# Optimization experiments

Hardware: AMD Instinct MI355X
Metric: run time of the kernel (lower is better)

The kernel has to match this reference:

```python
import jax, jax.numpy as jnp
import numpy as np

# Model dims (match init_kwargs)
N_P, NV, P, S = 60, 5, 20, 14   # particles, vertices, pf features, sv features
HID, DE, DO, NCLS, BATCH = 60, 20, 24, 2, 512

# Rr/Rs one-hot matrices encode edges (r, s) for r != s with r varying slowest.
# So gather-by-Rr == repeat each node N-1 times, gather-by-Rs == index by senders,
# and scatter-sum by Rr^T == reshape to [B, N, N-1, De] and sum axis 2.
_SENDERS = np.array([s for r in range(N_P) for s in range(N_P) if s != r])


def _lin_params(key, din, dout):
    kw, kb = jax.random.split(key)
    bound = 1.0 / np.sqrt(din)
    w = jax.random.uniform(kw, (din, dout), minval=-bound, maxval=bound, dtype=jnp.float32)
    b = jax.random.uniform(kb, (dout,), minval=-bound, maxval=bound, dtype=jnp.float32)
    return w, b


def setup_inputs() -> dict:
    key = jax.random.key(0)
    ks = jax.random.split(key, 12)
    inp = {
        'x': jax.random.normal(ks[0], (BATCH, P, N_P), dtype=jnp.float32),
        'y': jax.random.normal(ks[1], (BATCH, S, NV), dtype=jnp.float32),
    }
    specs = [('fr', [(2 * P, HID), (HID, HID), (HID, DE)]),
             ('pv', [(S + P, HID), (HID, HID), (HID, DE)]),
             ('fo', [(P + 2 * DE, HID), (HID, HID), (HID, DO)])]
    ki = 2
    for name, dims in specs:
        for j, (di, do) in enumerate(dims, 1):
            w, b = _lin_params(ks[ki], di, do)
            ki += 1
            inp[f'{name}_w{j}'] = w
            inp[f'{name}_b{j}'] = b
    w, b = _lin_params(ks[11], DO, NCLS)
    inp['fc_w'] = w
    inp['fc_b'] = b
    return inp


def _mlp3(h, w1, b1, w2, b2, w3, b3):
    h = jax.nn.relu(h @ w1 + b1)
    h = jax.nn.relu(h @ w2 + b2)
    return jax.nn.relu(h @ w3 + b3)


def reference(x, y, fr_w1, fr_b1, fr_w2, fr_b2, fr_w3, fr_b3,
              pv_w1, pv_b1, pv_w2, pv_b2, pv_w3, pv_b3,
              fo_w1, fo_b1, fo_w2, fo_b2, fo_w3, fo_b3, fc_w, fc_b):
    xt = jnp.swapaxes(x, -1, -2)  # [B, N, P]
    yt = jnp.swapaxes(y, -1, -2)  # [B, Nv, S]
    B = xt.shape[0]

    # particle-particle edge conv (gather via index, scatter-sum via reshape)
    Orr = jnp.repeat(xt, N_P - 1, axis=1)          # [B, Nr, P], receiver features
    Ors = xt[:, _SENDERS]                          # [B, Nr, P], sender features
    E = _mlp3(jnp.concatenate([Orr, Ors], axis=-1),
              fr_w1, fr_b1, fr_w2, fr_b2, fr_w3, fr_b3)  # [B, Nr, De]
    Ebar_pp = E.reshape(B, N_P, N_P - 1, DE).sum(axis=2)  # [B, N, De]

    # particle-vertex edge conv (Rk repeats particles, Rv tiles vertices)
    Ork = jnp.repeat(xt, NV, axis=1)               # [B, Nt, P]
    Orv = jnp.tile(yt, (1, N_P, 1))                # [B, Nt, S]
    E2 = _mlp3(jnp.concatenate([Ork, Orv], axis=-1),
               pv_w1, pv_b1, pv_w2, pv_b2, pv_w3, pv_b3)  # [B, Nt, De]
    Ebar_pv = E2.reshape(B, N_P, NV, DE).sum(axis=2)      # [B, N, De]

    C = jnp.concatenate([xt, Ebar_pp, Ebar_pv], axis=-1)  # [B, N, P + 2*De]
    O = _mlp3(C, fo_w1, fo_b1, fo_w2, fo_b2, fo_w3, fo_b3)  # [B, N, Do]
    return O.sum(axis=-2) @ fc_w + fc_b  # [B, num_classes]
```

## Files before the change

### kernel.cpp

```cpp
#include <hip/hip_runtime.h>

#define BATCH 512
#define NPART 60
#define PFEAT 20
#define SFEAT 14
#define NVTX  5
#define HID   60
#define DE    20
#define DO    24
#define NCLS  2
#define SR    68

typedef _Float16 half8  __attribute__((ext_vector_type(8)));
typedef _Float16 half4v __attribute__((ext_vector_type(4)));
typedef __fp16   fp16x2 __attribute__((ext_vector_type(2)));
typedef float    f32x4  __attribute__((ext_vector_type(4)));

__device__ __forceinline__ half4v pkcvt4(f32x4 a) {
    fp16x2 lo = __builtin_amdgcn_cvt_pkrtz(a[0], a[1]);
    fp16x2 hi = __builtin_amdgcn_cvt_pkrtz(a[2], a[3]);
    half4v r;
    r[0] = (_Float16)lo[0]; r[1] = (_Float16)lo[1];
    r[2] = (_Float16)hi[0]; r[3] = (_Float16)hi[1];
    return r;
}
__device__ __forceinline__ half4v relu4(half4v a) {
#pragma unroll
    for (int j = 0; j < 4; ++j)
        a[j] = (a[j] > (_Float16)0.f) ? a[j] : (_Float16)0.f;
    return a;
}

__global__ __launch_bounds__(256) void prep_kernel(
    const float* __restrict__ x,
    const float* __restrict__ fr_w1, const float* __restrict__ fr_b1,
    const float* __restrict__ pv_w1,
    const float* __restrict__ fr_w2, const float* __restrict__ fr_b2,
    const float* __restrict__ fr_w3, const float* __restrict__ fr_b3,
    const float* __restrict__ pv_w2, const float* __restrict__ pv_b2,
    const float* __restrict__ pv_w3, const float* __restrict__ pv_b3,
    const float* __restrict__ fo_w1, const float* __restrict__ fo_b1,
    const float* __restrict__ fo_w2, const float* __restrict__ fo_b2,
    const float* __restrict__ fo_w3, const float* __restrict__ fo_b3,
    _Float16* __restrict__ frW2p, _Float16* __restrict__ frW3p16,
    _Float16* __restrict__ pvW2p, _Float16* __restrict__ pvW3p16,
    _Float16* __restrict__ foW1p, _Float16* __restrict__ foW2p16,
    _Float16* __restrict__ foW3p16,
    _Float16* __restrict__ frW1Ap, _Float16* __restrict__ frW1Bp,
    _Float16* __restrict__ pvW1Ap, _Float16* __restrict__ xp)
{
    if (blockIdx.x < 16) {
        int idx = blockIdx.x*256 + threadIdx.x;
        {
            int j  = idx & 7;
            int L  = (idx >> 3) & 63;
            int kk = (idx >> 9) & 1;
            int u  = idx >> 10;
            int k  = kk*32 + (L >> 4)*8 + j;
            int n  = u*16 + (L & 15);
            float v2f = 0.f, v2p = 0.f, v1o = 0.f;
            if (k < HID && n < HID) {
                v2f = fr_w2[k*HID + n];
                v2p = pv_w2[k*HID + n];
                v1o = fo_w1[k*HID + n];
            } else if (k == HID) {
                if (n < HID)      { v2f = fr_b2[n]; v2p = pv_b2[n]; v1o = fo_b1[n]; }
                else if (n == HID){ v2f = 1.f;      v2p = 1.f;      v1o = 1.f; }
            }
            frW2p[idx] = (_Float16)v2f;
            pvW2p[idx] = (_Float16)v2p;
            foW1p[idx] = (_Float16)v1o;
        }
        {
            int j  = idx & 3;
            int L  = (idx >> 2) & 63;
            int kt = (idx >> 8) & 3;
            int u  = idx >> 10;
            int k  = kt*16 + (L >> 4)*4 + j;
            int n  = u*16 + (L & 15);
            float v = 0.f;
            if (k < HID && n < HID)        v = fo_w2[k*HID + n];
            else if (k == HID) {
                if (n < HID)       v = fo_b2[n];
                else if (n == HID) v = 1.f;
            }
            foW2p16[idx] = (_Float16)v;
        }
        if (idx < 2048) {
            {
                int j  = idx & 3;
                int L  = (idx >> 2) & 63;
                int kt = (idx >> 8) & 3;
                int u  = idx >> 10;
                int k  = kt*16 + (L >> 4)*4 + j;
                int n  = u*16 + (L & 15);
                float vf = 0.f, vp = 0.f, vo = 0.f;
                if (k < HID) {
                    if (n < DE) { vf = fr_w3[k*DE + n]; vp = pv_w3[k*DE + n]; }
                    if (n < DO)   vo = fo_w3[k*DO + n];
                } else if (k == HID) {
                    if (n < DE) { vf = fr_b3[n]; vp = pv_b3[n]; }
                    if (n < DO)   vo = fo_w3 ? fo_b3[n] : 0.f;
                }
                frW3p16[idx] = (_Float16)vf;
                pvW3p16[idx] = (_Float16)vp;
                foW3p16[idx] = (_Float16)vo;
            }
            {
                int j = idx & 7;
                int L = (idx >> 3) & 63;
                int u = idx >> 9;
                int k = (L >> 4)*8 + j;
                int n = u*16 + (L & 15);
                float va = 0.f, vb = 0.f, vpv = 0.f;
                if (k < PFEAT && n < HID) {
                    va  = fr_w1[k*HID + n];
                    vb  = fr_w1[(PFEAT + k)*HID + n];
                    vpv = pv_w1[k*HID + n];
                } else if (k == PFEAT) {
                    if (n < HID)       va = fr_b1[n];
                    else if (n == HID) va = 1.f;
                }
                frW1Ap[idx] = (_Float16)va;
                frW1Bp[idx] = (_Float16)vb;
                pvW1Ap[idx] = (_Float16)vpv;
            }
        }
    } else {
        int idx = (blockIdx.x - 16)*256 + threadIdx.x;
        if (idx < BATCH*NPART*4) {
            int p = idx % NPART;
            int t = idx / NPART;
            int q = t & 3;
            int b = t >> 2;
            half8 v;
#pragma unroll
            for (int j = 0; j < 8; ++j) {
                int k = q*8 + j;
                float f = 0.f;
                if (k < PFEAT)       f = x[((size_t)b*PFEAT + k)*NPART + p];
                else if (k == PFEAT) f = 1.f;
                v[j] = (_Float16)f;
            }
            *(half8*)(xp + (size_t)idx*8) = v;
        }
    }
}

__global__ __launch_bounds__(512) void fused_kernel(
    const float* __restrict__ y,
    const float* __restrict__ pv_w1, const float* __restrict__ pv_b1,
    const float* __restrict__ fcw, const float* __restrict__ fcb,
    const half8*  __restrict__ frw2p, const half4v* __restrict__ frw3p16,
    const half8*  __restrict__ pvw2p, const half4v* __restrict__ pvw3p16,
    const half8*  __restrict__ fow1p, const half4v* __restrict__ fow2p16,
    const half4v* __restrict__ fow3p16,
    const half8*  __restrict__ frw1ap, const half8* __restrict__ frw1bp,
    const half8*  __restrict__ pvw1ap, const _Float16* __restrict__ xp,
    float* __restrict__ out)
{
    __shared__ __align__(16) _Float16 sFrA[NPART*SR];
    __shared__ __align__(16) _Float16 sFrB[NPART*SR];
    __shared__ __align__(16) _Float16 sPvA[NPART*SR];
    __shared__ __align__(16) _Float16 sPvV[NVTX*64];
    __shared__ __align__(16) _Float16 sEpp[NPART*DE];
    __shared__ __align__(16) _Float16 sEpvP[NVTX*NPART*DE];
    __shared__ __align__(16) float    sDsum[4][DO];
    _Float16* sCin = sFrA;

    const f32x4 z4 = {0.f, 0.f, 0.f, 0.f};

    int bb   = blockIdx.x;
    int wv   = threadIdx.x >> 6;
    int lane = threadIdx.x & 63;
    int ml   = lane & 15;
    int q    = lane >> 4;

    {
        int tile = wv & 3;
        int row  = 16*tile + ml;
        int rr   = (row < NPART) ? row : 0;
        half8 bX = *(const half8*)(xp + (((size_t)bb*4 + q)*NPART + rr)*8);
#pragma unroll
        for (int task = 0; task < 2; ++task) {
            const half8* Wt; _Float16* Ot;
            if (wv < 4) {
                if (task == 0) { Wt = frw1ap; Ot = sFrA; }
                else           { Wt = pvw1ap; Ot = sPvA; }
            } else {
                if (task == 1) break;
                Wt = frw1bp; Ot = sFrB;
            }
#pragma unroll
            for (int u = 0; u < 4; ++u) {
                half8 w8 = Wt[u*64 + lane];
                f32x4 acc = z4;
                acc = __builtin_amdgcn_mfma_f32_16x16x32_f16(w8, bX, acc, 0, 0, 0);
                if (row < NPART)
                    *(half4v*)(Ot + row*SR + u*16 + 4*q) = pkcvt4(acc);
            }
        }
        for (int idx = threadIdx.x; idx < NVTX*64; idx += 512) {
            int v = idx >> 6;
            int h = idx & 63;
            float a;
            if (h < HID) {
                a = pv_b1[h];
#pragma unroll
                for (int f = 0; f < SFEAT; ++f)
                    a += y[((size_t)bb*SFEAT + f)*NVTX + v] * pv_w1[(PFEAT + f)*HID + h];
            } else {
                a = (h == HID) ? 1.f : 0.f;
            }
            sPvV[idx] = (_Float16)a;
        }
    }
    __syncthreads();

    {
        half8  w2r[8];
        half4v w3r[8];
#pragma unroll
        for (int t = 0; t < 8; ++t) w2r[t] = frw2p[t*64 + lane];
#pragma unroll
        for (int t = 0; t < 8; ++t) w3r[t] = frw3p16[t*64 + lane];
#pragma unroll
        for (int t = 0; t < 8; ++t) {
            asm volatile("" : "+v"(w2r[t]));
            asm volatile("" : "+v"(w3r[t]));
        }
        float ok3[4];
#pragma unroll
        for (int i = 0; i < 4; ++i) ok3[i] = (4*q + i < 11) ? 1.f : 0.f;

        for (int r = wv; r < NPART; r += 8) {
            half8 u8k0 = *(const half8*)(sFrA + r*SR + q*8);
            half8 u8k1 = *(const half8*)(sFrA + r*SR + 32 + q*8);
            float s0 = 0.f, s1 = 0.f;

#pragma unroll
            for (int c = 0; c < 4; ++c) {
                int edge = 16*c + ml;
                bool eok = (edge < NPART-1);
                int sr = eok ? (edge + (edge >= r)) : 0;
                half8 bA0, bA1;
                {
                    half8 v8 = *(const half8*)(sFrB + sr*SR + q*8);
                    half8 s8 = u8k0 + v8;
#pragma unroll
                    for (int j = 0; j < 8; ++j)
                        s8[j] = (s8[j] > (_Float16)0.f) ? s8[j] : (_Float16)0.f;
                    bA0 = s8;
                    v8 = *(const half8*)(sFrB + sr*SR + 32 + q*8);
                    s8 = u8k1 + v8;
#pragma unroll
                    for (int j = 0; j < 8; ++j)
                        s8[j] = (s8[j] > (_Float16)0.f) ? s8[j] : (_Float16)0.f;
                    bA1 = s8;
                }
                half4v a3u[4];
#pragma unroll
                for (int u = 0; u < 4; ++u) {
                    f32x4 a = z4;
                    a = __builtin_amdgcn_mfma_f32_16x16x32_f16(w2r[u*2 + 0], bA0, a, 0, 0, 0);
                    a = __builtin_amdgcn_mfma_f32_16x16x32_f16(w2r[u*2 + 1], bA1, a, 0, 0, 0);
                    a3u[u] = relu4(pkcvt4(a));
                }
                f32x4 e0 = z4, e1 = z4;
#pragma unroll
                for (int u = 0; u < 4; ++u) {
                    e0 = __builtin_amdgcn_mfma_f32_16x16x16f16(a3u[u], w3r[0*4 + u], e0, 0, 0, 0);
                    e1 = __builtin_amdgcn_mfma_f32_16x16x16f16(a3u[u], w3r[1*4 + u], e1, 0, 0, 0);
                }
                if (c < 3) {
#pragma unroll
                    for (int i = 0; i < 4; ++i) {
                        s0 += fmaxf(e0[i], 0.f);
                        s1 += fmaxf(e1[i], 0.f);
                    }
                } else {
#pragma unroll
                    for (int i = 0; i < 4; ++i) {
                        s0 = fmaf(fmaxf(e0[i], 0.f), ok3[i], s0);
                        s1 = fmaf(fmaxf(e1[i], 0.f), ok3[i], s1);
                    }
                }
            }
            s0 += __shfl_xor(s0, 16);
            s1 += __shfl_xor(s1, 16);
            s0 += __shfl_xor(s0, 32);
            s1 += __shfl_xor(s1, 32);
            if (q == 0) {
                sEpp[r*DE + ml] = (_Float16)s0;
                if (ml < DE - 16)
                    sEpp[r*DE + 16 + ml] = (_Float16)s1;
            }
        }
    }

    if (wv < NVTX) {
        int gv = wv;
        half8  w2r[8];
        half4v w3r[8];
#pragma unroll
        for (int t = 0; t < 8; ++t) w2r[t] = pvw2p[t*64 + lane];
#pragma unroll
        for (int t = 0; t < 8; ++t) w3r[t] = pvw3p16[t*64 + lane];
#pragma unroll
        for (int t = 0; t < 8; ++t) {
            asm volatile("" : "+v"(w2r[t]));
            asm volatile("" : "+v"(w3r[t]));
        }
        half8 u8k0 = *(const half8*)(sPvV + gv*64 + q*8);
        half8 u8k1 = *(const half8*)(sPvV + gv*64 + 32 + q*8);
#pragma unroll
        for (int th = 0; th < 2; ++th) {
            half8 bA[2][2];
#pragma unroll
            for (int tl = 0; tl < 2; ++tl) {
                int p = 16*(2*th + tl) + ml;
                int sr = (p < NPART) ? p : 0;
#pragma unroll
                for (int kk = 0; kk < 2; ++kk) {
                    half8 v8 = *(const half8*)(sPvA + sr*SR + kk*32 + q*8);
                    half8 s8 = (kk ? u8k1 : u8k0) + v8;
#pragma unroll
                    for (int j = 0; j < 8; ++j) {
                        _Float16 vj = s8[j];
                        s8[j] = (vj > (_Float16)0.f) ? vj : (_Float16)0.f;
                    }
                    bA[tl][kk] = s8;
                }
            }
            f32x4 acc3[2][2];
#pragma unroll
            for (int v = 0; v < 2; ++v)
#pragma unroll
                for (int tl = 0; tl < 2; ++tl) acc3[v][tl] = z4;
#pragma unroll
            for (int u = 0; u < 4; ++u) {
                half8 w0 = w2r[u*2 + 0];
                half8 w1 = w2r[u*2 + 1];
                half4v a3u[2];
#pragma unroll
                for (int tl = 0; tl < 2; ++tl) {
                    f32x4 a = z4;
                    a = __builtin_amdgcn_mfma_f32_16x16x32_f16(w0, bA[tl][0], a, 0, 0, 0);
                    a = __builtin_amdgcn_mfma_f32_16x16x32_f16(w1, bA[tl][1], a, 0, 0, 0);
                    a3u[tl] = relu4(pkcvt4(a));
                }
                half4v w3a = w3r[0*4 + u];
                half4v w3b = w3r[1*4 + u];
#pragma unroll
                for (int tl = 0; tl < 2; ++tl) {
                    acc3[0][tl] = __builtin_amdgcn_mfma_f32_16x16x16f16(w3a, a3u[tl], acc3[0][tl], 0, 0, 0);
                    acc3[1][tl] = __builtin_amdgcn_mfma_f32_16x16x16f16(w3b, a3u[tl], acc3[1][tl], 0, 0, 0);
                }
            }
#pragma unroll
            for (int v = 0; v < 2; ++v) {
                int col4 = v*16 + 4*q;
#pragma unroll
                for (int tl = 0; tl < 2; ++tl) {
                    int p = 16*(2*th + tl) + ml;
                    if (p < NPART && col4 < DE) {
                        half4v hv = relu4(pkcvt4(acc3[v][tl]));
                        *(half4v*)(sEpvP + (gv*NPART + p)*DE + col4) = hv;
                    }
                }
            }
        }
    }
    __syncthreads();

    for (int idx = threadIdx.x; idx < NPART*64; idx += 512) {
        int p = idx >> 6;
        int k = idx & 63;
        _Float16 v;
        if (k < PFEAT) {
            v = xp[(((size_t)bb*4 + (k >> 3))*NPART + p)*8 + (k & 7)];
        } else if (k < PFEAT + DE) {
            v = sEpp[p*DE + (k - PFEAT)];
        } else if (k < PFEAT + 2*DE) {
            int c = k - PFEAT - DE;
            float s = 0.f;
#pragma unroll
            for (int g5 = 0; g5 < NVTX; ++g5)
                s += (float)sEpvP[(g5*NPART + p)*DE + c];
            v = (_Float16)s;
        } else {
            v = (k == HID) ? (_Float16)1.f : (_Float16)0.f;
        }
        sCin[p*SR + k] = v;
    }
    __syncthreads();

    if (wv < 4) {
        int p = 16*wv + ml;
        int sp = (p < NPART) ? p : 0;
        half8 bC[2];
#pragma unroll
        for (int kk = 0; kk < 2; ++kk)
            bC[kk] = *(const half8*)(sCin + sp*SR + kk*32 + q*8);

        f32x4 acc1[4];
#pragma unroll
        for (int u = 0; u < 4; ++u) {
            acc1[u] = z4;
            acc1[u] = __builtin_amdgcn_mfma_f32_16x16x32_f16(fow1p[(u*2 + 0)*64 + lane], bC[0], acc1[u], 0, 0, 0);
            acc1[u] = __builtin_amdgcn_mfma_f32_16x16x32_f16(fow1p[(u*2 + 1)*64 + lane], bC[1], acc1[u], 0, 0, 0);
        }
        half4v a2[4];
#pragma unroll
        for (int u = 0; u < 4; ++u) a2[u] = relu4(pkcvt4(acc1[u]));

        f32x4 acc2[4];
#pragma unroll
        for (int u = 0; u < 4; ++u) {
            acc2[u] = z4;
#pragma unroll
            for (int kt = 0; kt < 4; ++kt)
                acc2[u] = __builtin_amdgcn_mfma_f32_16x16x16f16(fow2p16[(u*4 + kt)*64 + lane], a2[kt], acc2[u], 0, 0, 0);
        }
        half4v a3[4];
#pragma unroll
        for (int u = 0; u < 4; ++u) a3[u] = relu4(pkcvt4(acc2[u]));

        f32x4 e0 = z4, e1 = z4;
#pragma unroll
        for (int u = 0; u < 4; ++u) {
            e0 = __builtin_amdgcn_mfma_f32_16x16x16f16(a3[u], fow3p16[(0*4 + u)*64 + lane], e0, 0, 0, 0);
            e1 = __builtin_amdgcn_mfma_f32_16x16x16f16(a3[u], fow3p16[(1*4 + u)*64 + lane], e1, 0, 0, 0);
        }
        float okp = (wv < 3 || q < 3) ? 1.f : 0.f;
        float s0 = 0.f, s1 = 0.f;
#pragma unroll
        for (int i = 0; i < 4; ++i) {
            s0 += fmaxf(e0[i], 0.f);
            s1 += fmaxf(e1[i], 0.f);
        }
        s0 *= okp; s1 *= okp;
        s0 += __shfl_xor(s0, 16);
        s1 += __shfl_xor(s1, 16);
        s0 += __shfl_xor(s0, 32);
        s1 += __shfl_xor(s1, 32);
        if (q == 0) {
            sDsum[wv][ml] = s0;
            if (ml < DO - 16)
                sDsum[wv][16 + ml] = s1;
        }
    }
    __syncthreads();

    if (wv == 0) {
        float tot = 0.f;
        if (lane < DO) {
#pragma unroll
            for (int w4 = 0; w4 < 4; ++w4) tot += sDsum[w4][lane];
        }
        float p0 = (lane < DO) ? tot * fcw[lane*NCLS + 0] : 0.f;
        float p1 = (lane < DO) ? tot * fcw[lane*NCLS + 1] : 0.f;
#pragma unroll
        for (int d = 1; d <= 16; d <<= 1) {
            p0 += __shfl_xor(p0, d);
            p1 += __shfl_xor(p1, d);
        }
        if (lane == 0) {
            out[bb*NCLS + 0] = p0 + fcb[0];
            out[bb*NCLS + 1] = p1 + fcb[1];
        }
    }
}

extern "C" void kernel_launch(void* const* d_in, const int* in_sizes, int n_in,
                              void* d_out, int out_size, void* d_ws, size_t ws_size,
                              hipStream_t stream)
{
    const float* x     = (const float*)d_in[0];
    const float* y     = (const float*)d_in[1];
    const float* fr_w1 = (const float*)d_in[2];
    const float* fr_b1 = (const float*)d_in[3];
    const float* fr_w2 = (const float*)d_in[4];
    const float* fr_b2 = (const float*)d_in[5];
    const float* fr_w3 = (const float*)d_in[6];
    const float* fr_b3 = (const float*)d_in[7];
    const float* pv_w1 = (const float*)d_in[8];
    const float* pv_b1 = (const float*)d_in[9];
    const float* pv_w2 = (const float*)d_in[10];
    const float* pv_b2 = (const float*)d_in[11];
    const float* pv_w3 = (const float*)d_in[12];
    const float* pv_b3 = (const float*)d_in[13];
    const float* fo_w1 = (const float*)d_in[14];
    const float* fo_b1 = (const float*)d_in[15];
    const float* fo_w2 = (const float*)d_in[16];
    const float* fo_b2 = (const float*)d_in[17];
    const float* fo_w3 = (const float*)d_in[18];
    const float* fo_b3 = (const float*)d_in[19];
    const float* fc_w  = (const float*)d_in[20];
    const float* fc_b  = (const float*)d_in[21];
    float* out = (float*)d_out;

    char* wsb = (char*)d_ws;
    size_t off = 0;
    auto alloc = [&](size_t bytes) { char* p = wsb + off; off += (bytes + 255) & ~(size_t)255; return p; };

    _Float16* frW2p   = (_Float16*)alloc(4096*2);
    _Float16* frW3p16 = (_Float16*)alloc(2048*2);
    _Float16* pvW2p   = (_Float16*)alloc(4096*2);
    _Float16* pvW3p16 = (_Float16*)alloc(2048*2);
    _Float16* foW1p   = (_Float16*)alloc(4096*2);
    _Float16* foW2p16 = (_Float16*)alloc(4096*2);
    _Float16* foW3p16 = (_Float16*)alloc(2048*2);
    _Float16* frW1Ap  = (_Float16*)alloc(2048*2);
    _Float16* frW1Bp  = (_Float16*)alloc(2048*2);
    _Float16* pvW1Ap  = (_Float16*)alloc(2048*2);
    _Float16* xp      = (_Float16*)alloc((size_t)BATCH*NPART*32*2);

    int xblocks = (BATCH*NPART*4 + 255)/256;
    prep_kernel<<<16 + xblocks, 256, 0, stream>>>(
        x, fr_w1, fr_b1, pv_w1,
        fr_w2, fr_b2, fr_w3, fr_b3,
        pv_w2, pv_b2, pv_w3, pv_b3,
        fo_w1, fo_b1, fo_w2, fo_b2, fo_w3, fo_b3,
        frW2p, frW3p16, pvW2p, pvW3p16, foW1p, foW2p16, foW3p16,
        frW1Ap, frW1Bp, pvW1Ap, xp);

    fused_kernel<<<BATCH, 512, 0, stream>>>(
        y, pv_w1, pv_b1, fc_w, fc_b,
        (const half8*)frW2p, (const half4v*)frW3p16,
        (const half8*)pvW2p, (const half4v*)pvW3p16,
        (const half8*)foW1p, (const half4v*)foW2p16, (const half4v*)foW3p16,
        (const half8*)frW1Ap, (const half8*)frW1Bp,
        (const half8*)pvW1Ap, xp,
        out);
}
```

Measured before the change: 131.4 us.

## Split each batch item across two blocks by receiver halves, add head kernel

Each batch element now runs in two workgroups, each handling 30 of the 60 receiver particles for the edge, vertex and output MLPs. The per-half partial sums go to a workspace buffer, and a new small kernel combines them and applies the final linear layer. This doubles the grid to expose more parallelism on the GPU and reduces shared memory per block. In exchange, every block recomputes the full sender projection and the vertex layer, and the change adds a third kernel launch.

Measured after the change: 137.2 us. 4.4% more time.

```diff
diff --git a/kernel.cpp b/kernel.cpp
--- a/kernel.cpp
+++ b/kernel.cpp
@@ -10,6 +10,7 @@
 #define DO    24
 #define NCLS  2
 #define SR    68
+#define RPB   30
 
 typedef _Float16 half8  __attribute__((ext_vector_type(8)));
 typedef _Float16 half4v __attribute__((ext_vector_type(4)));
@@ -100,7 +101,7 @@
                     if (n < DO)   vo = fo_w3[k*DO + n];
                 } else if (k == HID) {
                     if (n < DE) { vf = fr_b3[n]; vp = pv_b3[n]; }
-                    if (n < DO)   vo = fo_w3 ? fo_b3[n] : 0.f;
+                    if (n < DO)   vo = fo_b3[n];
                 }
                 frW3p16[idx] = (_Float16)vf;
                 pvW3p16[idx] = (_Float16)vp;
@@ -150,55 +151,49 @@
 __global__ __launch_bounds__(512) void fused_kernel(
     const float* __restrict__ y,
     const float* __restrict__ pv_w1, const float* __restrict__ pv_b1,
-    const float* __restrict__ fcw, const float* __restrict__ fcb,
     const half8*  __restrict__ frw2p, const half4v* __restrict__ frw3p16,
     const half8*  __restrict__ pvw2p, const half4v* __restrict__ pvw3p16,
     const half8*  __restrict__ fow1p, const half4v* __restrict__ fow2p16,
     const half4v* __restrict__ fow3p16,
     const half8*  __restrict__ frw1ap, const half8* __restrict__ frw1bp,
     const half8*  __restrict__ pvw1ap, const _Float16* __restrict__ xp,
-    float* __restrict__ out)
+    float* __restrict__ pdsum)
 {
-    __shared__ __align__(16) _Float16 sFrA[NPART*SR];
+    __shared__ __align__(16) _Float16 sFrA[32*SR];
     __shared__ __align__(16) _Float16 sFrB[NPART*SR];
-    __shared__ __align__(16) _Float16 sPvA[NPART*SR];
+    __shared__ __align__(16) _Float16 sPvA[32*SR];
     __shared__ __align__(16) _Float16 sPvV[NVTX*64];
-    __shared__ __align__(16) _Float16 sEpp[NPART*DE];
-    __shared__ __align__(16) _Float16 sEpvP[NVTX*NPART*DE];
-    __shared__ __align__(16) float    sDsum[4][DO];
+    __shared__ __align__(16) _Float16 sEpp[32*DE];
+    __shared__ __align__(16) _Float16 sEpvP[NVTX*32*DE];
+    __shared__ __align__(16) float    sDsum[2][DO];
     _Float16* sCin = sFrA;
 
     const f32x4 z4 = {0.f, 0.f, 0.f, 0.f};
 
-    int bb   = blockIdx.x;
+    int bid  = blockIdx.x;
+    int bb   = bid >> 1;
+    int half = bid & 1;
+    int base = half * RPB;
     int wv   = threadIdx.x >> 6;
     int lane = threadIdx.x & 63;
     int ml   = lane & 15;
     int q    = lane >> 4;
 
     {
-        int tile = wv & 3;
-        int row  = 16*tile + ml;
-        int rr   = (row < NPART) ? row : 0;
+        const half8* Wt; _Float16* Ot; int lr, row; bool ok;
+        if (wv < 2)      { Wt = frw1ap; Ot = sFrA; lr = 16*wv + ml;     row = base + lr; ok = (lr < RPB); }
+        else if (wv < 6) { Wt = frw1bp; Ot = sFrB; lr = 16*(wv-2) + ml; row = lr;        ok = (row < NPART); }
+        else             { Wt = pvw1ap; Ot = sPvA; lr = 16*(wv-6) + ml; row = base + lr; ok = (lr < RPB); }
+        int rr = ok ? row : 0;
+        int strow = (wv >= 2 && wv < 6) ? rr : ((lr < RPB) ? lr : 0);
         half8 bX = *(const half8*)(xp + (((size_t)bb*4 + q)*NPART + rr)*8);
 #pragma unroll
-        for (int task = 0; task < 2; ++task) {
-            const half8* Wt; _Float16* Ot;
-            if (wv < 4) {
-                if (task == 0) { Wt = frw1ap; Ot = sFrA; }
-                else           { Wt = pvw1ap; Ot = sPvA; }
-            } else {
-                if (task == 1) break;
-                Wt = frw1bp; Ot = sFrB;
-            }
-#pragma unroll
-            for (int u = 0; u < 4; ++u) {
-                half8 w8 = Wt[u*64 + lane];
-                f32x4 acc = z4;
-                acc = __builtin_amdgcn_mfma_f32_16x16x32_f16(w8, bX, acc, 0, 0, 0);
-                if (row < NPART)
-                    *(half4v*)(Ot + row*SR + u*16 + 4*q) = pkcvt4(acc);
-            }
+        for (int u = 0; u < 4; ++u) {
+            half8 w8 = Wt[u*64 + lane];
+            f32x4 acc = z4;
+            acc = __builtin_amdgcn_mfma_f32_16x16x32_f16(w8, bX, acc, 0, 0, 0);
+            if (ok)
+                *(half4v*)(Ot + strow*SR + u*16 + 4*q) = pkcvt4(acc);
         }
         for (int idx = threadIdx.x; idx < NVTX*64; idx += 512) {
             int v = idx >> 6;
@@ -233,9 +228,10 @@
 #pragma unroll
         for (int i = 0; i < 4; ++i) ok3[i] = (4*q + i < 11) ? 1.f : 0.f;
 
-        for (int r = wv; r < NPART; r += 8) {
-            half8 u8k0 = *(const half8*)(sFrA + r*SR + q*8);
-            half8 u8k1 = *(const half8*)(sFrA + r*SR + 32 + q*8);
+        for (int lr = wv; lr < RPB; lr += 8) {
+            int r = base + lr;
+            half8 u8k0 = *(const half8*)(sFrA + lr*SR + q*8);
+            half8 u8k1 = *(const half8*)(sFrA + lr*SR + 32 + q*8);
             float s0 = 0.f, s1 = 0.f;
 
 #pragma unroll
@@ -291,15 +287,15 @@
             s0 += __shfl_xor(s0, 32);
             s1 += __shfl_xor(s1, 32);
             if (q == 0) {
-                sEpp[r*DE + ml] = (_Float16)s0;
+                sEpp[lr*DE + ml] = (_Float16)s0;
                 if (ml < DE - 16)
-                    sEpp[r*DE + 16 + ml] = (_Float16)s1;
-            }
-        }
-    }
-
-    if (wv < NVTX) {
-        int gv = wv;
+                    sEpp[lr*DE + 16 + ml] = (_Float16)s1;
+            }
+        }
+    }
+
+    if (wv >= 3) {
+        int gv = wv - 3;
         half8  w2r[8];
         half4v w3r[8];
 #pragma unroll
@@ -313,91 +309,89 @@
         }
         half8 u8k0 = *(const half8*)(sPvV + gv*64 + q*8);
         half8 u8k1 = *(const half8*)(sPvV + gv*64 + 32 + q*8);
-#pragma unroll
-        for (int th = 0; th < 2; ++th) {
-            half8 bA[2][2];
+
+        half8 bA[2][2];
+#pragma unroll
+        for (int tl = 0; tl < 2; ++tl) {
+            int lp = 16*tl + ml;
+            int sp = (lp < RPB) ? lp : 0;
+#pragma unroll
+            for (int kk = 0; kk < 2; ++kk) {
+                half8 v8 = *(const half8*)(sPvA + sp*SR + kk*32 + q*8);
+                half8 s8 = (kk ? u8k1 : u8k0) + v8;
+#pragma unroll
+                for (int j = 0; j < 8; ++j) {
+                    _Float16 vj = s8[j];
+                    s8[j] = (vj > (_Float16)0.f) ? vj : (_Float16)0.f;
+                }
+                bA[tl][kk] = s8;
+            }
+        }
+        f32x4 acc3[2][2];
+#pragma unroll
+        for (int v = 0; v < 2; ++v)
+#pragma unroll
+            for (int tl = 0; tl < 2; ++tl) acc3[v][tl] = z4;
+#pragma unroll
+        for (int u = 0; u < 4; ++u) {
+            half8 w0 = w2r[u*2 + 0];
+            half8 w1 = w2r[u*2 + 1];
+            half4v a3u[2];
 #pragma unroll
             for (int tl = 0; tl < 2; ++tl) {
-                int p = 16*(2*th + tl) + ml;
-                int sr = (p < NPART) ? p : 0;
-#pragma unroll
-                for (int kk = 0; kk < 2; ++kk) {
-                    half8 v8 = *(const half8*)(sPvA + sr*SR + kk*32 + q*8);
-                    half8 s8 = (kk ? u8k1 : u8k0) + v8;
-#pragma unroll
-                    for (int j = 0; j < 8; ++j) {
-                        _Float16 vj = s8[j];
-                        s8[j] = (vj > (_Float16)0.f) ? vj : (_Float16)0.f;
-                    }
-                    bA[tl][kk] = s8;
-                }
-            }
-            f32x4 acc3[2][2];
-#pragma unroll
-            for (int v = 0; v < 2; ++v)
-#pragma unroll
-                for (int tl = 0; tl < 2; ++tl) acc3[v][tl] = z4;
-#pragma unroll
-            for (int u = 0; u < 4; ++u) {
-                half8 w0 = w2r[u*2 + 0];
-                half8 w1 = w2r[u*2 + 1];
-                half4v a3u[2];
-#pragma unroll
-                for (int tl = 0; tl < 2; ++tl) {
-                    f32x4 a = z4;
-                    a = __builtin_amdgcn_mfma_f32_16x16x32_f16(w0, bA[tl][0], a, 0, 0, 0);
-                    a = __builtin_amdgcn_mfma_f32_16x16x32_f16(w1, bA[tl][1], a, 0, 0, 0);
-                    a3u[tl] = relu4(pkcvt4(a));
-                }
-                half4v w3a = w3r[0*4 + u];
-                half4v w3b = w3r[1*4 + u];
-#pragma unroll
-                for (int tl = 0; tl < 2; ++tl) {
-                    acc3[0][tl] = __builtin_amdgcn_mfma_f32_16x16x16f16(w3a, a3u[tl], acc3[0][tl], 0, 0, 0);
-                    acc3[1][tl] = __builtin_amdgcn_mfma_f32_16x16x16f16(w3b, a3u[tl], acc3[1][tl], 0, 0, 0);
-                }
-            }
-#pragma unroll
-            for (int v = 0; v < 2; ++v) {
-                int col4 = v*16 + 4*q;
-#pragma unroll
-                for (int tl = 0; tl < 2; ++tl) {
-                    int p = 16*(2*th + tl) + ml;
-                    if (p < NPART && col4 < DE) {
-                        half4v hv = relu4(pkcvt4(acc3[v][tl]));
-                        *(half4v*)(sEpvP + (gv*NPART + p)*DE + col4) = hv;
-                    }
+                f32x4 a = z4;
+                a = __builtin_amdgcn_mfma_f32_16x16x32_f16(w0, bA[tl][0], a, 0, 0, 0);
+                a = __builtin_amdgcn_mfma_f32_16x16x32_f16(w1, bA[tl][1], a, 0, 0, 0);
+                a3u[tl] = relu4(pkcvt4(a));
+            }
+            half4v w3a = w3r[0*4 + u];
+            half4v w3b = w3r[1*4 + u];
+#pragma unroll
+            for (int tl = 0; tl < 2; ++tl) {
+                acc3[0][tl] = __builtin_amdgcn_mfma_f32_16x16x16f16(w3a, a3u[tl], acc3[0][tl], 0, 0, 0);
+                acc3[1][tl] = __builtin_amdgcn_mfma_f32_16x16x16f16(w3b, a3u[tl], acc3[1][tl], 0, 0, 0);
+            }
+        }
+#pragma unroll
+        for (int v = 0; v < 2; ++v) {
+            int col4 = v*16 + 4*q;
+#pragma unroll
+            for (int tl = 0; tl < 2; ++tl) {
+                int lp = 16*tl + ml;
+                if (lp < RPB && col4 < DE) {
+                    half4v hv = relu4(pkcvt4(acc3[v][tl]));
+                    *(half4v*)(sEpvP + (gv*32 + lp)*DE + col4) = hv;
                 }
             }
         }
     }
     __syncthreads();
 
-    for (int idx = threadIdx.x; idx < NPART*64; idx += 512) {
-        int p = idx >> 6;
-        int k = idx & 63;
+    for (int idx = threadIdx.x; idx < RPB*64; idx += 512) {
+        int lp = idx >> 6;
+        int k  = idx & 63;
         _Float16 v;
         if (k < PFEAT) {
-            v = xp[(((size_t)bb*4 + (k >> 3))*NPART + p)*8 + (k & 7)];
+            v = xp[(((size_t)bb*4 + (k >> 3))*NPART + base + lp)*8 + (k & 7)];
         } else if (k < PFEAT + DE) {
-            v = sEpp[p*DE + (k - PFEAT)];
+            v = sEpp[lp*DE + (k - PFEAT)];
         } else if (k < PFEAT + 2*DE) {
             int c = k - PFEAT - DE;
             float s = 0.f;
 #pragma unroll
             for (int g5 = 0; g5 < NVTX; ++g5)
-                s += (float)sEpvP[(g5*NPART + p)*DE + c];
+                s += (float)sEpvP[(g5*32 + lp)*DE + c];
             v = (_Float16)s;
         } else {
             v = (k == HID) ? (_Float16)1.f : (_Float16)0.f;
         }
-        sCin[p*SR + k] = v;
+        sCin[lp*SR + k] = v;
     }
     __syncthreads();
 
-    if (wv < 4) {
-        int p = 16*wv + ml;
-        int sp = (p < NPART) ? p : 0;
+    if (wv < 2) {
+        int lp = 16*wv + ml;
+        int sp = (lp < RPB) ? lp : 0;
         half8 bC[2];
 #pragma unroll
         for (int kk = 0; kk < 2; ++kk)
@@ -432,14 +426,13 @@
             e0 = __builtin_amdgcn_mfma_f32_16x16x16f16(a3[u], fow3p16[(0*4 + u)*64 + lane], e0, 0, 0, 0);
             e1 = __builtin_amdgcn_mfma_f32_16x16x16f16(a3[u], fow3p16[(1*4 + u)*64 + lane], e1, 0, 0, 0);
         }
-        float okp = (wv < 3 || q < 3) ? 1.f : 0.f;
         float s0 = 0.f, s1 = 0.f;
 #pragma unroll
         for (int i = 0; i < 4; ++i) {
-            s0 += fmaxf(e0[i], 0.f);
-            s1 += fmaxf(e1[i], 0.f);
-        }
-        s0 *= okp; s1 *= okp;
+            float okp = (16*wv + 4*q + i < RPB) ? 1.f : 0.f;
+            s0 = fmaf(fmaxf(e0[i], 0.f), okp, s0);
+            s1 = fmaf(fmaxf(e1[i], 0.f), okp, s1);
+        }
         s0 += __shfl_xor(s0, 16);
         s1 += __shfl_xor(s1, 16);
         s0 += __shfl_xor(s0, 32);
@@ -452,24 +445,25 @@
     }
     __syncthreads();
 
-    if (wv == 0) {
-        float tot = 0.f;
-        if (lane < DO) {
-#pragma unroll
-            for (int w4 = 0; w4 < 4; ++w4) tot += sDsum[w4][lane];
-        }
-        float p0 = (lane < DO) ? tot * fcw[lane*NCLS + 0] : 0.f;
-        float p1 = (lane < DO) ? tot * fcw[lane*NCLS + 1] : 0.f;
-#pragma unroll
-        for (int d = 1; d <= 16; d <<= 1) {
-            p0 += __shfl_xor(p0, d);
-            p1 += __shfl_xor(p1, d);
-        }
-        if (lane == 0) {
-            out[bb*NCLS + 0] = p0 + fcb[0];
-            out[bb*NCLS + 1] = p1 + fcb[1];
-        }
-    }
+    if (wv == 0 && lane < DO) {
+        pdsum[((size_t)bb*2 + half)*DO + lane] = sDsum[0][lane] + sDsum[1][lane];
+    }
+}
+
+__global__ __launch_bounds__(256) void head_kernel(
+    const float* __restrict__ pdsum, const float* __restrict__ fcw,
+    const float* __restrict__ fcb, float* __restrict__ out)
+{
+    int i = blockIdx.x*256 + threadIdx.x;
+    if (i >= BATCH*NCLS) return;
+    int bb = i >> 1;
+    int c  = i & 1;
+    const float* p0 = pdsum + (size_t)bb*2*DO;
+    float s = fcb[c];
+#pragma unroll
+    for (int d = 0; d < DO; ++d)
+        s += (p0[d] + p0[DO + d]) * fcw[d*NCLS + c];
+    out[i] = s;
 }
 
 extern "C" void kernel_launch(void* const* d_in, const int* in_sizes, int n_in,
@@ -515,6 +509,7 @@
     _Float16* frW1Bp  = (_Float16*)alloc(2048*2);
     _Float16* pvW1Ap  = (_Float16*)alloc(2048*2);
     _Float16* xp      = (_Float16*)alloc((size_t)BATCH*NPART*32*2);
+    float*    pdsum   = (float*)alloc((size_t)BATCH*2*DO*sizeof(float));
 
     int xblocks = (BATCH*NPART*4 + 255)/256;
     prep_kernel<<<16 + xblocks, 256, 0, stream>>>(
@@ -525,12 +520,14 @@
         frW2p, frW3p16, pvW2p, pvW3p16, foW1p, foW2p16, foW3p16,
         frW1Ap, frW1Bp, pvW1Ap, xp);
 
-    fused_kernel<<<BATCH, 512, 0, stream>>>(
-        y, pv_w1, pv_b1, fc_w, fc_b,
+    fused_kernel<<<BATCH*2, 512, 0, stream>>>(
+        y, pv_w1, pv_b1,
         (const half8*)frW2p, (const half4v*)frW3p16,
         (const half8*)pvW2p, (const half4v*)pvW3p16,
         (const half8*)foW1p, (const half4v*)foW2p16, (const half4v*)foW3p16,
         (const half8*)frW1Ap, (const half8*)frW1Bp,
         (const half8*)pvW1Ap, xp,
-        out);
+        pdsum);
+
+    head_kernel<<<(BATCH*NCLS + 255)/256, 256, 0, stream>>>(pdsum, fc_w, fc_b, out);
 }
```

## Precompute vertex projection in prep kernel, rebalance PV waves, MFMA-based reductions

Applied to the files above, without the earlier changes.

Moves the per-batch vertex-feature projection (y times pv_w1 plus bias) out of the fused kernel into extra blocks of the prep kernel, writing fp16 to workspace. The particle-vertex edge MLP is now split into 20 smaller work units spread over the upper four waves instead of five waves doing larger tiles, which is meant to balance work against the particle-particle waves. Cross-lane sums of ReLU outputs are replaced by an MFMA against a ones matrix instead of shuffles. The MFMA sum rounds partial values to fp16 first, which loses some precision, and the extra workspace round trip adds global traffic.

Result: slower. 134.4 us (+2.3%).

```diff
diff --git a/kernel.cpp b/kernel.cpp
--- a/kernel.cpp
+++ b/kernel.cpp
@@ -32,9 +32,9 @@
 }
 
 __global__ __launch_bounds__(256) void prep_kernel(
-    const float* __restrict__ x,
+    const float* __restrict__ x, const float* __restrict__ y,
     const float* __restrict__ fr_w1, const float* __restrict__ fr_b1,
-    const float* __restrict__ pv_w1,
+    const float* __restrict__ pv_w1, const float* __restrict__ pv_b1,
     const float* __restrict__ fr_w2, const float* __restrict__ fr_b2,
     const float* __restrict__ fr_w3, const float* __restrict__ fr_b3,
     const float* __restrict__ pv_w2, const float* __restrict__ pv_b2,
@@ -47,7 +47,8 @@
     _Float16* __restrict__ foW1p, _Float16* __restrict__ foW2p16,
     _Float16* __restrict__ foW3p16,
     _Float16* __restrict__ frW1Ap, _Float16* __restrict__ frW1Bp,
-    _Float16* __restrict__ pvW1Ap, _Float16* __restrict__ xp)
+    _Float16* __restrict__ pvW1Ap, _Float16* __restrict__ xp,
+    _Float16* __restrict__ pvvp)
 {
     if (blockIdx.x < 16) {
         int idx = blockIdx.x*256 + threadIdx.x;
@@ -100,7 +101,7 @@
                     if (n < DO)   vo = fo_w3[k*DO + n];
                 } else if (k == HID) {
                     if (n < DE) { vf = fr_b3[n]; vp = pv_b3[n]; }
-                    if (n < DO)   vo = fo_w3 ? fo_b3[n] : 0.f;
+                    if (n < DO)   vo = fo_b3[n];
                 }
                 frW3p16[idx] = (_Float16)vf;
                 pvW3p16[idx] = (_Float16)vp;
@@ -126,7 +127,7 @@
                 pvW1Ap[idx] = (_Float16)vpv;
             }
         }
-    } else {
+    } else if (blockIdx.x < 16 + 480) {
         int idx = (blockIdx.x - 16)*256 + threadIdx.x;
         if (idx < BATCH*NPART*4) {
             int p = idx % NPART;
@@ -144,12 +145,28 @@
             }
             *(half8*)(xp + (size_t)idx*8) = v;
         }
+    } else {
+        int idx = (blockIdx.x - (16 + 480))*256 + threadIdx.x;
+        if (idx < BATCH*NVTX*64) {
+            int h = idx & 63;
+            int t = idx >> 6;
+            int v = t % NVTX;
+            int b = t / NVTX;
+            float a;
+            if (h < HID) {
+                a = pv_b1[h];
+#pragma unroll
+                for (int f = 0; f < SFEAT; ++f)
+                    a += y[((size_t)b*SFEAT + f)*NVTX + v] * pv_w1[(PFEAT + f)*HID + h];
+            } else {
+                a = (h == HID) ? 1.f : 0.f;
+            }
+            pvvp[idx] = (_Float16)a;
+        }
     }
 }
 
 __global__ __launch_bounds__(512) void fused_kernel(
-    const float* __restrict__ y,
-    const float* __restrict__ pv_w1, const float* __restrict__ pv_b1,
     const float* __restrict__ fcw, const float* __restrict__ fcb,
     const half8*  __restrict__ frw2p, const half4v* __restrict__ frw3p16,
     const half8*  __restrict__ pvw2p, const half4v* __restrict__ pvw3p16,
@@ -157,12 +174,12 @@
     const half4v* __restrict__ fow3p16,
     const half8*  __restrict__ frw1ap, const half8* __restrict__ frw1bp,
     const half8*  __restrict__ pvw1ap, const _Float16* __restrict__ xp,
+    const half8*  __restrict__ pvvp,
     float* __restrict__ out)
 {
     __shared__ __align__(16) _Float16 sFrA[NPART*SR];
     __shared__ __align__(16) _Float16 sFrB[NPART*SR];
     __shared__ __align__(16) _Float16 sPvA[NPART*SR];
-    __shared__ __align__(16) _Float16 sPvV[NVTX*64];
     __shared__ __align__(16) _Float16 sEpp[NPART*DE];
     __shared__ __align__(16) _Float16 sEpvP[NVTX*NPART*DE];
     __shared__ __align__(16) float    sDsum[4][DO];
@@ -175,6 +192,10 @@
     int lane = threadIdx.x & 63;
     int ml   = lane & 15;
     int q    = lane >> 4;
+
+    half4v onesA;
+#pragma unroll
+    for (int j = 0; j < 4; ++j) onesA[j] = (_Float16)1.f;
 
     {
         int tile = wv & 3;
@@ -200,20 +221,6 @@
                     *(half4v*)(Ot + row*SR + u*16 + 4*q) = pkcvt4(acc);
             }
         }
-        for (int idx = threadIdx.x; idx < NVTX*64; idx += 512) {
-            int v = idx >> 6;
-            int h = idx & 63;
-            float a;
-            if (h < HID) {
-                a = pv_b1[h];
-#pragma unroll
-                for (int f = 0; f < SFEAT; ++f)
-                    a += y[((size_t)bb*SFEAT + f)*NVTX + v] * pv_w1[(PFEAT + f)*HID + h];
-            } else {
-                a = (h == HID) ? 1.f : 0.f;
-            }
-            sPvV[idx] = (_Float16)a;
-        }
     }
     __syncthreads();
 
@@ -229,20 +236,19 @@
             asm volatile("" : "+v"(w2r[t]));
             asm volatile("" : "+v"(w3r[t]));
         }
-        float ok3[4];
-#pragma unroll
-        for (int i = 0; i < 4; ++i) ok3[i] = (4*q + i < 11) ? 1.f : 0.f;
+        half4v m3;
+#pragma unroll
+        for (int j = 0; j < 4; ++j) m3[j] = (_Float16)((4*q + j < 11) ? 1.f : 0.f);
 
         for (int r = wv; r < NPART; r += 8) {
             half8 u8k0 = *(const half8*)(sFrA + r*SR + q*8);
             half8 u8k1 = *(const half8*)(sFrA + r*SR + 32 + q*8);
-            float s0 = 0.f, s1 = 0.f;
+            f32x4 accS0 = z4, accS1 = z4;
 
 #pragma unroll
             for (int c = 0; c < 4; ++c) {
                 int edge = 16*c + ml;
-                bool eok = (edge < NPART-1);
-                int sr = eok ? (edge + (edge >= r)) : 0;
+                int sr = (edge < NPART-1) ? (edge + (edge >= r)) : 0;
                 half8 bA0, bA1;
                 {
                     half8 v8 = *(const half8*)(sFrB + sr*SR + q*8);
@@ -272,34 +278,21 @@
                     e0 = __builtin_amdgcn_mfma_f32_16x16x16f16(a3u[u], w3r[0*4 + u], e0, 0, 0, 0);
                     e1 = __builtin_amdgcn_mfma_f32_16x16x16f16(a3u[u], w3r[1*4 + u], e1, 0, 0, 0);
                 }
-                if (c < 3) {
-#pragma unroll
-                    for (int i = 0; i < 4; ++i) {
-                        s0 += fmaxf(e0[i], 0.f);
-                        s1 += fmaxf(e1[i], 0.f);
-                    }
-                } else {
-#pragma unroll
-                    for (int i = 0; i < 4; ++i) {
-                        s0 = fmaf(fmaxf(e0[i], 0.f), ok3[i], s0);
-                        s1 = fmaf(fmaxf(e1[i], 0.f), ok3[i], s1);
-                    }
-                }
-            }
-            s0 += __shfl_xor(s0, 16);
-            s1 += __shfl_xor(s1, 16);
-            s0 += __shfl_xor(s0, 32);
-            s1 += __shfl_xor(s1, 32);
+                half4v p0 = relu4(pkcvt4(e0));
+                half4v p1 = relu4(pkcvt4(e1));
+                if (c == 3) { p0 *= m3; p1 *= m3; }
+                accS0 = __builtin_amdgcn_mfma_f32_16x16x16f16(onesA, p0, accS0, 0, 0, 0);
+                accS1 = __builtin_amdgcn_mfma_f32_16x16x16f16(onesA, p1, accS1, 0, 0, 0);
+            }
             if (q == 0) {
-                sEpp[r*DE + ml] = (_Float16)s0;
+                sEpp[r*DE + ml] = (_Float16)accS0[0];
                 if (ml < DE - 16)
-                    sEpp[r*DE + 16 + ml] = (_Float16)s1;
-            }
-        }
-    }
-
-    if (wv < NVTX) {
-        int gv = wv;
+                    sEpp[r*DE + 16 + ml] = (_Float16)accS1[0];
+            }
+        }
+    }
+
+    if (wv >= 4) {
         half8  w2r[8];
         half4v w3r[8];
 #pragma unroll
@@ -311,62 +304,44 @@
             asm volatile("" : "+v"(w2r[t]));
             asm volatile("" : "+v"(w3r[t]));
         }
-        half8 u8k0 = *(const half8*)(sPvV + gv*64 + q*8);
-        half8 u8k1 = *(const half8*)(sPvV + gv*64 + 32 + q*8);
-#pragma unroll
-        for (int th = 0; th < 2; ++th) {
-            half8 bA[2][2];
-#pragma unroll
-            for (int tl = 0; tl < 2; ++tl) {
-                int p = 16*(2*th + tl) + ml;
-                int sr = (p < NPART) ? p : 0;
-#pragma unroll
-                for (int kk = 0; kk < 2; ++kk) {
-                    half8 v8 = *(const half8*)(sPvA + sr*SR + kk*32 + q*8);
-                    half8 s8 = (kk ? u8k1 : u8k0) + v8;
-#pragma unroll
-                    for (int j = 0; j < 8; ++j) {
-                        _Float16 vj = s8[j];
-                        s8[j] = (vj > (_Float16)0.f) ? vj : (_Float16)0.f;
-                    }
-                    bA[tl][kk] = s8;
-                }
-            }
-            f32x4 acc3[2][2];
-#pragma unroll
-            for (int v = 0; v < 2; ++v)
-#pragma unroll
-                for (int tl = 0; tl < 2; ++tl) acc3[v][tl] = z4;
+        for (int kunit = wv - 4; kunit < 20; kunit += 4) {
+            int gv = kunit >> 2;
+            int tl = kunit & 3;
+            int p  = 16*tl + ml;
+            int sp = (p < NPART) ? p : 0;
+            const half8* pvvB = pvvp + ((size_t)bb*NVTX + gv)*8;
+            half8 u8k0 = pvvB[q];
+            half8 u8k1 = pvvB[4 + q];
+
+            half8 bA[2];
+#pragma unroll
+            for (int kk = 0; kk < 2; ++kk) {
+                half8 v8 = *(const half8*)(sPvA + sp*SR + kk*32 + q*8);
+                half8 s8 = (kk ? u8k1 : u8k0) + v8;
+#pragma unroll
+                for (int j = 0; j < 8; ++j) {
+                    _Float16 vj = s8[j];
+                    s8[j] = (vj > (_Float16)0.f) ? vj : (_Float16)0.f;
+                }
+                bA[kk] = s8;
+            }
+            f32x4 acc3[2];
+            acc3[0] = z4; acc3[1] = z4;
 #pragma unroll
             for (int u = 0; u < 4; ++u) {
-                half8 w0 = w2r[u*2 + 0];
-                half8 w1 = w2r[u*2 + 1];
-                half4v a3u[2];
-#pragma unroll
-                for (int tl = 0; tl < 2; ++tl) {
-                    f32x4 a = z4;
-                    a = __builtin_amdgcn_mfma_f32_16x16x32_f16(w0, bA[tl][0], a, 0, 0, 0);
-                    a = __builtin_amdgcn_mfma_f32_16x16x32_f16(w1, bA[tl][1], a, 0, 0, 0);
-                    a3u[tl] = relu4(pkcvt4(a));
-                }
-                half4v w3a = w3r[0*4 + u];
-                half4v w3b = w3r[1*4 + u];
-#pragma unroll
-                for (int tl = 0; tl < 2; ++tl) {
-                    acc3[0][tl] = __builtin_amdgcn_mfma_f32_16x16x16f16(w3a, a3u[tl], acc3[0][tl], 0, 0, 0);
-                    acc3[1][tl] = __builtin_amdgcn_mfma_f32_16x16x16f16(w3b, a3u[tl], acc3[1][tl], 0, 0, 0);
-                }
+                f32x4 a = z4;
+                a = __builtin_amdgcn_mfma_f32_16x16x32_f16(w2r[u*2 + 0], bA[0], a, 0, 0, 0);
+                a = __builtin_amdgcn_mfma_f32_16x16x32_f16(w2r[u*2 + 1], bA[1], a, 0, 0, 0);
+                half4v a3u = relu4(pkcvt4(a));
+                acc3[0] = __builtin_amdgcn_mfma_f32_16x16x16f16(w3r[0*4 + u], a3u, acc3[0], 0, 0, 0);
+                acc3[1] = __builtin_amdgcn_mfma_f32_16x16x16f16(w3r[1*4 + u], a3u, acc3[1], 0, 0, 0);
             }
 #pragma unroll
             for (int v = 0; v < 2; ++v) {
                 int col4 = v*16 + 4*q;
-#pragma unroll
-                for (int tl = 0; tl < 2; ++tl) {
-                    int p = 16*(2*th + tl) + ml;
-                    if (p < NPART && col4 < DE) {
-                        half4v hv = relu4(pkcvt4(acc3[v][tl]));
-                        *(half4v*)(sEpvP + (gv*NPART + p)*DE + col4) = hv;
-                    }
+                if (p < NPART && col4 < DE) {
+                    half4v hv = relu4(pkcvt4(acc3[v]));
+                    *(half4v*)(sEpvP + (gv*NPART + p)*DE + col4) = hv;
                 }
             }
         }
@@ -432,22 +407,18 @@
             e0 = __builtin_amdgcn_mfma_f32_16x16x16f16(a3[u], fow3p16[(0*4 + u)*64 + lane], e0, 0, 0, 0);
             e1 = __builtin_amdgcn_mfma_f32_16x16x16f16(a3[u], fow3p16[(1*4 + u)*64 + lane], e1, 0, 0, 0);
         }
-        float okp = (wv < 3 || q < 3) ? 1.f : 0.f;
-        float s0 = 0.f, s1 = 0.f;
-#pragma unroll
-        for (int i = 0; i < 4; ++i) {
-            s0 += fmaxf(e0[i], 0.f);
-            s1 += fmaxf(e1[i], 0.f);
-        }
-        s0 *= okp; s1 *= okp;
-        s0 += __shfl_xor(s0, 16);
-        s1 += __shfl_xor(s1, 16);
-        s0 += __shfl_xor(s0, 32);
-        s1 += __shfl_xor(s1, 32);
+        half4v p0 = relu4(pkcvt4(e0));
+        half4v p1 = relu4(pkcvt4(e1));
+        if (wv == 3 && q == 3) {
+#pragma unroll
+            for (int j = 0; j < 4; ++j) { p0[j] = (_Float16)0.f; p1[j] = (_Float16)0.f; }
+        }
+        f32x4 accP0 = __builtin_amdgcn_mfma_f32_16x16x16f16(onesA, p0, z4, 0, 0, 0);
+        f32x4 accP1 = __builtin_amdgcn_mfma_f32_16x16x16f16(onesA, p1, z4, 0, 0, 0);
         if (q == 0) {
-            sDsum[wv][ml] = s0;
+            sDsum[wv][ml] = accP0[0];
             if (ml < DO - 16)
-                sDsum[wv][16 + ml] = s1;
+                sDsum[wv][16 + ml] = accP1[0];
         }
     }
     __syncthreads();
@@ -515,22 +486,24 @@
     _Float16* frW1Bp  = (_Float16*)alloc(2048*2);
     _Float16* pvW1Ap  = (_Float16*)alloc(2048*2);
     _Float16* xp      = (_Float16*)alloc((size_t)BATCH*NPART*32*2);
-
-    int xblocks = (BATCH*NPART*4 + 255)/256;
-    prep_kernel<<<16 + xblocks, 256, 0, stream>>>(
-        x, fr_w1, fr_b1, pv_w1,
+    _Float16* pvvp    = (_Float16*)alloc((size_t)BATCH*NVTX*64*2);
+
+    int xblocks  = (BATCH*NPART*4 + 255)/256;
+    int pvblocks = (BATCH*NVTX*64 + 255)/256;
+    prep_kernel<<<16 + xblocks + pvblocks, 256, 0, stream>>>(
+        x, y, fr_w1, fr_b1, pv_w1, pv_b1,
         fr_w2, fr_b2, fr_w3, fr_b3,
         pv_w2, pv_b2, pv_w3, pv_b3,
         fo_w1, fo_b1, fo_w2, fo_b2, fo_w3, fo_b3,
         frW2p, frW3p16, pvW2p, pvW3p16, foW1p, foW2p16, foW3p16,
-        frW1Ap, frW1Bp, pvW1Ap, xp);
+        frW1Ap, frW1Bp, pvW1Ap, xp, pvvp);
 
     fused_kernel<<<BATCH, 512, 0, stream>>>(
-        y, pv_w1, pv_b1, fc_w, fc_b,
+        fc_w, fc_b,
         (const half8*)frW2p, (const half4v*)frW3p16,
         (const half8*)pvW2p, (const half4v*)pvW3p16,
         (const half8*)foW1p, (const half4v*)foW2p16, (const half4v*)foW3p16,
         (const half8*)frW1Ap, (const half8*)frW1Bp,
-        (const half8*)pvW1Ap, xp,
+        (const half8*)pvW1Ap, xp, (const half8*)pvvp,
         out);
 }
```
